# Kernel tuning notes

Hardware: AMD Instinct MI355X
Metric: run time of the kernel (lower is better)

The kernel has to match this reference:

```python
import jax, jax.numpy as jnp
import numpy as np

B, L, H = 8, 4096, 1024


def setup_inputs() -> dict:
    key = jax.random.key(0)
    k1, k2 = jax.random.split(key)
    sequence_output = jax.random.normal(k1, (B, L, H), dtype=jnp.float32)
    # each wordpiece position maps to the token it belongs to (monotone non-decreasing)
    wordpiece_to_token = jnp.sort(
        jax.random.randint(k2, (B, L), 0, L, dtype=jnp.int32), axis=-1
    )
    return {"sequence_output": sequence_output, "wordpiece_to_token": wordpiece_to_token}


def reference(sequence_output, wordpiece_to_token):
    # output[b, t, :] = sum over wordpieces w with wordpiece_to_token[b, w] == t
    b_, l_, h_ = sequence_output.shape
    # offset segment ids per batch element so one flat segment_sum handles all
    seg = (wordpiece_to_token.astype(jnp.int32) + jnp.arange(b_, dtype=jnp.int32)[:, None] * l_)
    out = jax.ops.segment_sum(
        sequence_output.reshape(b_ * l_, h_), seg.reshape(-1), num_segments=b_ * l_
    )
    return out.reshape(b_, l_, h_)
```

## Files before the change

### kernel.cpp

```cpp
#include <hip/hip_runtime.h>
#include <hip/hip_bf16.h>


#define B_DIM 8
#define L_DIM 4096
#define H_DIM 1024
#define LP1   (L_DIM + 1)

__global__ __launch_bounds__(256) void build_starts_kernel(
    const int* __restrict__ tok,
    int* __restrict__ start)
{
    const int gid = blockIdx.x * 256 + threadIdx.x;
    const int b = gid >> 12;
    const int w = gid & (L_DIM - 1);

    const int* __restrict__ row = tok + (size_t)b * L_DIM;
    const int cur  = row[w];
    const int prev = (w > 0) ? row[w - 1] : -1;

    int* __restrict__ srow = start + (size_t)b * LP1;
    for (int t = prev + 1; t <= cur; ++t) srow[t] = w;
    if (w == L_DIM - 1) {
        for (int t = cur + 1; t <= L_DIM; ++t) srow[t] = L_DIM;
    }
}

__global__ __launch_bounds__(256) void token_seg_sum_kernel(
    const float* __restrict__ seq,
    const int* __restrict__ start,
    float* __restrict__ out)
{
    const int bt = blockIdx.x;
    const int b  = bt >> 12;
    const int t  = bt & (L_DIM - 1);

    const int* __restrict__ srow = start + (size_t)b * LP1;
    const int s = srow[t];
    const int e = srow[t + 1];

    const int tid = threadIdx.x;
    const float4* __restrict__ base =
        (const float4*)(seq + (size_t)b * L_DIM * H_DIM);

    float4 acc = make_float4(0.f, 0.f, 0.f, 0.f);
    for (int w = s; w < e; ++w) {
        float4 v = base[(size_t)w * (H_DIM / 4) + tid];
        acc.x += v.x; acc.y += v.y; acc.z += v.z; acc.w += v.w;
    }

    ((float4*)out)[(size_t)bt * (H_DIM / 4) + tid] = acc;
}

extern "C" void kernel_launch(void* const* d_in, const int* in_sizes, int n_in,
                              void* d_out, int out_size, void* d_ws, size_t ws_size,
                              hipStream_t stream) {
    const float* seq = (const float*)d_in[0];
    const int*   tok = (const int*)d_in[1];
    float*       out = (float*)d_out;
    int*         start = (int*)d_ws;

    build_starts_kernel<<<dim3(B_DIM * L_DIM / 256), dim3(256), 0, stream>>>(tok, start);
    token_seg_sum_kernel<<<dim3(B_DIM * L_DIM), dim3(256), 0, stream>>>(seq, start, out);
}
```

Baseline: 230.2 us.

## Assign four consecutive tokens per wavefront in segment-sum kernel

The one-block-per-token mapping is replaced by one 64-lane wavefront per group of four consecutive tokens. Each lane handles four float4 columns of the hidden row, and the grid shrinks by a factor of 16. The goal is to cut block-launch overhead and the many near-empty blocks (about a third of tokens are empty), and to get more independent loads in flight per thread. The trade-off is that work per wavefront now varies with segment lengths, which can cause load imbalance. The start-offset row stride is padded to L+8 so each wavefront can read its five boundary offsets.

Result: slower. 243.5 us (+5.8%).

```diff
diff --git a/kernel.cpp b/kernel.cpp
--- a/kernel.cpp
+++ b/kernel.cpp
@@ -1,11 +1,11 @@
 #include <hip/hip_runtime.h>
-#include <hip/hip_bf16.h>
 
 
 #define B_DIM 8
 #define L_DIM 4096
 #define H_DIM 1024
-#define LP1   (L_DIM + 1)
+#define LSTRIDE (L_DIM + 8)
+#define TPW 4
 
 __global__ __launch_bounds__(256) void build_starts_kernel(
     const int* __restrict__ tok,
@@ -19,11 +19,15 @@
     const int cur  = row[w];
     const int prev = (w > 0) ? row[w - 1] : -1;
 
-    int* __restrict__ srow = start + (size_t)b * LP1;
+    int* __restrict__ srow = start + (size_t)b * LSTRIDE;
     for (int t = prev + 1; t <= cur; ++t) srow[t] = w;
     if (w == L_DIM - 1) {
         for (int t = cur + 1; t <= L_DIM; ++t) srow[t] = L_DIM;
     }
+}
+
+__device__ __forceinline__ void acc4(float4& a, const float4 v) {
+    a.x += v.x; a.y += v.y; a.z += v.z; a.w += v.w;
 }
 
 __global__ __launch_bounds__(256) void token_seg_sum_kernel(
@@ -31,25 +35,42 @@
     const int* __restrict__ start,
     float* __restrict__ out)
 {
-    const int bt = blockIdx.x;
-    const int b  = bt >> 12;
-    const int t  = bt & (L_DIM - 1);
+    const int wid   = (blockIdx.x << 2) | (threadIdx.x >> 6);
+    const int lane  = threadIdx.x & 63;
+    const int tglob = wid * TPW;
+    const int b     = tglob >> 12;
+    const int t0    = tglob & (L_DIM - 1);
 
-    const int* __restrict__ srow = start + (size_t)b * LP1;
-    const int s = srow[t];
-    const int e = srow[t + 1];
+    const int* __restrict__ srow = start + b * LSTRIDE + t0;
+    int st[TPW + 1];
+#pragma unroll
+    for (int i = 0; i <= TPW; ++i) st[i] = srow[i];
 
-    const int tid = threadIdx.x;
-    const float4* __restrict__ base =
-        (const float4*)(seq + (size_t)b * L_DIM * H_DIM);
+    const float4* __restrict__ base  = (const float4*)seq + ((size_t)b << 20);
+    float4* __restrict__       obase = (float4*)out + ((size_t)tglob << 8);
 
-    float4 acc = make_float4(0.f, 0.f, 0.f, 0.f);
-    for (int w = s; w < e; ++w) {
-        float4 v = base[(size_t)w * (H_DIM / 4) + tid];
-        acc.x += v.x; acc.y += v.y; acc.z += v.z; acc.w += v.w;
+#pragma unroll
+    for (int i = 0; i < TPW; ++i) {
+        float4 a0 = make_float4(0.f, 0.f, 0.f, 0.f);
+        float4 a1 = a0, a2 = a0, a3 = a0;
+
+        const int s = st[i];
+        const int e = st[i + 1];
+        for (int w = s; w < e; ++w) {
+            const float4* __restrict__ r = base + ((size_t)w << 8) + lane;
+            float4 v0 = r[0];
+            float4 v1 = r[64];
+            float4 v2 = r[128];
+            float4 v3 = r[192];
+            acc4(a0, v0); acc4(a1, v1); acc4(a2, v2); acc4(a3, v3);
+        }
+
+        float4* __restrict__ o = obase + (i << 8) + lane;
+        o[0]   = a0;
+        o[64]  = a1;
+        o[128] = a2;
+        o[192] = a3;
     }
-
-    ((float4*)out)[(size_t)bt * (H_DIM / 4) + tid] = acc;
 }
 
 extern "C" void kernel_launch(void* const* d_in, const int* in_sizes, int n_in,
@@ -61,5 +82,7 @@
     int*         start = (int*)d_ws;
 
     build_starts_kernel<<<dim3(B_DIM * L_DIM / 256), dim3(256), 0, stream>>>(tok, start);
-    token_seg_sum_kernel<<<dim3(B_DIM * L_DIM), dim3(256), 0, stream>>>(seq, start, out);
+
+    token_seg_sum_kernel<<<dim3(B_DIM * L_DIM / (TPW * 4)), dim3(256), 0, stream>>>(
+        seq, start, out);
 }
```

## Fuse start-index build into a wordpiece-chunked segment-sum kernel with streaming stores

Applied to the files above, without the earlier changes.

Removes the separate kernel that built per-token start offsets. Each block now handles a chunk of 8 consecutive wordpieces, loading all 8 rows up front, and uses the sorted token ids to sum runs directly. It writes zeros for empty tokens in the gaps and extends the last run past the chunk boundary. Output stores are nontemporal. The aim is to drop a launch and an indirection, raise memory-level parallelism per block, and avoid cache pollution from the large output. In exchange, a run crossing a chunk boundary is read again by the block that owns its start, and long runs of empty tokens are zeroed serially by one block.

Result: slower. 238.3 us (+3.5%).

```diff
diff --git a/kernel.cpp b/kernel.cpp
--- a/kernel.cpp
+++ b/kernel.cpp
@@ -1,55 +1,72 @@
 #include <hip/hip_runtime.h>
-#include <hip/hip_bf16.h>
 
 
 #define B_DIM 8
 #define L_DIM 4096
 #define H_DIM 1024
-#define LP1   (L_DIM + 1)
+#define RPW 8
+#define SPB (L_DIM / RPW)
 
-__global__ __launch_bounds__(256) void build_starts_kernel(
-    const int* __restrict__ tok,
-    int* __restrict__ start)
-{
-    const int gid = blockIdx.x * 256 + threadIdx.x;
-    const int b = gid >> 12;
-    const int w = gid & (L_DIM - 1);
-
-    const int* __restrict__ row = tok + (size_t)b * L_DIM;
-    const int cur  = row[w];
-    const int prev = (w > 0) ? row[w - 1] : -1;
-
-    int* __restrict__ srow = start + (size_t)b * LP1;
-    for (int t = prev + 1; t <= cur; ++t) srow[t] = w;
-    if (w == L_DIM - 1) {
-        for (int t = cur + 1; t <= L_DIM; ++t) srow[t] = L_DIM;
-    }
-}
+typedef float fx4 __attribute__((ext_vector_type(4)));
 
 __global__ __launch_bounds__(256) void token_seg_sum_kernel(
     const float* __restrict__ seq,
-    const int* __restrict__ start,
+    const int* __restrict__ tok,
     float* __restrict__ out)
 {
-    const int bt = blockIdx.x;
-    const int b  = bt >> 12;
-    const int t  = bt & (L_DIM - 1);
-
-    const int* __restrict__ srow = start + (size_t)b * LP1;
-    const int s = srow[t];
-    const int e = srow[t + 1];
+    const int g  = blockIdx.x;
+    const int b  = g / SPB;
+    const int r0 = (g % SPB) * RPW;
 
     const int tid = threadIdx.x;
-    const float4* __restrict__ base =
-        (const float4*)(seq + (size_t)b * L_DIM * H_DIM);
+    const fx4* __restrict__ base = (const fx4*)seq + ((size_t)b << 20) + tid;
+    fx4* __restrict__ obase      = (fx4*)out + ((size_t)b << 20) + tid;
+    const int* __restrict__ trow = tok + ((size_t)b << 12);
 
-    float4 acc = make_float4(0.f, 0.f, 0.f, 0.f);
-    for (int w = s; w < e; ++w) {
-        float4 v = base[(size_t)w * (H_DIM / 4) + tid];
-        acc.x += v.x; acc.y += v.y; acc.z += v.z; acc.w += v.w;
+    fx4 row[RPW];
+#pragma unroll
+    for (int r = 0; r < RPW; ++r)
+        row[r] = base[(size_t)(r0 + r) << 8];
+
+    int tk[RPW];
+#pragma unroll
+    for (int r = 0; r < RPW; ++r) tk[r] = trow[r0 + r];
+    const int jprev = (r0 == 0) ? -1 : trow[r0 - 1];
+
+    fx4 acc = (fx4)0.f;
+    int  prev    = jprev;
+    bool started = false;
+
+#pragma unroll
+    for (int r = 0; r < RPW; ++r) {
+        const int t = tk[r];
+        if (t != prev) {
+            if (started)
+                __builtin_nontemporal_store(acc, obase + ((size_t)prev << 8));
+            for (int j = prev + 1; j < t; ++j)
+                __builtin_nontemporal_store((fx4)0.f, obase + ((size_t)j << 8));
+            acc     = row[r];
+            prev    = t;
+            started = true;
+        } else if (started) {
+            acc += row[r];
+        }
     }
 
-    ((float4*)out)[(size_t)bt * (H_DIM / 4) + tid] = acc;
+    if (started) {
+        int w = r0 + RPW;
+        while (w < L_DIM && trow[w] == prev) {
+            acc += base[(size_t)w << 8];
+            ++w;
+        }
+        __builtin_nontemporal_store(acc, obase + ((size_t)prev << 8));
+    }
+
+    if (r0 + RPW == L_DIM) {
+        const int tlast = tk[RPW - 1];
+        for (int j = tlast + 1; j < L_DIM; ++j)
+            __builtin_nontemporal_store((fx4)0.f, obase + ((size_t)j << 8));
+    }
 }
 
 extern "C" void kernel_launch(void* const* d_in, const int* in_sizes, int n_in,
@@ -58,8 +75,8 @@
     const float* seq = (const float*)d_in[0];
     const int*   tok = (const int*)d_in[1];
     float*       out = (float*)d_out;
-    int*         start = (int*)d_ws;
+    (void)d_ws; (void)ws_size;
 
-    build_starts_kernel<<<dim3(B_DIM * L_DIM / 256), dim3(256), 0, stream>>>(tok, start);
-    token_seg_sum_kernel<<<dim3(B_DIM * L_DIM), dim3(256), 0, stream>>>(seq, start, out);
+    token_seg_sum_kernel<<<dim3(B_DIM * SPB), dim3(256), 0, stream>>>(
+        seq, tok, out);
 }
```
